# Optimization experiments

Measured on AMD Instinct MI355X. Metric: run time of the kernel, lower is better.

Reference implementation:

```python
import jax, jax.numpy as jnp
import numpy as np

S = 3000    # number of candidate spans (rows of g_i)
P = 80000   # total (mention, antecedent) pairs
GI = 768    # gi_dim
DD = 20     # distance/genre/speaker embedding dim
HID = 150   # mlp hidden dim (fixed in source)
ORDER = 2   # N: one higher-order refinement pass


def setup_inputs() -> dict:
    key = jax.random.key(0)
    ks = jax.random.split(key, 18)
    gij = 3 * GI + 3 * DD
    g_i = jax.random.normal(ks[0], (S, GI), jnp.float32)
    mention_scores = jax.random.normal(ks[1], (S, 1), jnp.float32)
    # sorted segment ids: ragged antecedent counts per mention, grouped contiguously
    mention_ids = jnp.sort(jax.random.randint(ks[2], (P,), 0, S, dtype=jnp.int32))
    antecedent_ids = jax.random.randint(ks[3], (P,), 0, S, dtype=jnp.int32)
    dist_bins = jax.random.randint(ks[4], (P,), 0, 10, dtype=jnp.int32)
    genre_ids = jax.random.randint(ks[5], (P,), 0, 7, dtype=jnp.int32) + 1   # 1..7, 0 is padding_idx
    speaker_ids = jax.random.randint(ks[6], (P,), 0, 2, dtype=jnp.int32) + 1  # 1..2, 0 is padding_idx
    w = lambda k, shp: 0.02 * jax.random.normal(k, shp, jnp.float32)
    dist_emb = w(ks[7], (10, DD))
    genre_emb = w(ks[8], (8, DD)).at[0].set(0.0)     # padding_idx=0
    speaker_emb = w(ks[9], (3, DD)).at[0].set(0.0)   # padding_idx=0
    W1 = w(ks[10], (gij, HID)); b1 = jnp.zeros((HID,), jnp.float32)
    W2 = w(ks[11], (HID, HID)); b2 = jnp.zeros((HID,), jnp.float32)
    W3 = w(ks[12], (HID, 1)); b3 = jnp.zeros((1,), jnp.float32)
    Wf = w(ks[13], (2 * GI, 1)); bf = jnp.zeros((1,), jnp.float32)
    return {"g_i": g_i, "mention_scores": mention_scores, "mention_ids": mention_ids,
            "antecedent_ids": antecedent_ids, "dist_bins": dist_bins, "genre_ids": genre_ids,
            "speaker_ids": speaker_ids, "dist_emb": dist_emb, "genre_emb": genre_emb,
            "speaker_emb": speaker_emb, "W1": W1, "b1": b1, "W2": W2, "b2": b2,
            "W3": W3, "b3": b3, "Wf": Wf, "bf": bf}


def _mlp(x, W1, b1, W2, b2, W3, b3):
    h = jax.nn.relu(x @ W1 + b1)
    h = jax.nn.relu(h @ W2 + b2)
    return h @ W3 + b3


def reference(g_i, mention_scores, mention_ids, antecedent_ids, dist_bins, genre_ids,
              speaker_ids, dist_emb, genre_emb, speaker_emb, W1, b1, W2, b2, W3, b3, Wf, bf):
    phi = jnp.concatenate([dist_emb[dist_bins], genre_emb[genre_ids], speaker_emb[speaker_ids]], axis=1)  # [P,60]
    seg = dict(num_segments=S, indices_are_sorted=True)
    g = g_i
    scores = None
    for n in range(ORDER):
        i_g = g[mention_ids]                # [P,GI] gather
        j_g = g[antecedent_ids]             # [P,GI] gather
        pairs = jnp.concatenate([i_g, j_g, i_g * j_g, phi], axis=1)  # [P,gij]
        scores = _mlp(pairs, W1, b1, W2, b2, W3, b3)                 # [P,1]
        if n < ORDER - 1:
            # higher_order_refinement: ragged segment softmax + weighted scatter update
            s = scores[:, 0]
            seg_max = jax.ops.segment_max(s, mention_ids, **seg)
            safe_max = jnp.where(jnp.isfinite(seg_max), seg_max, 0.0)
            e = jnp.exp(s - safe_max[mention_ids])
            denom = jax.ops.segment_sum(e, mention_ids, **seg)
            attn = e / jnp.where(denom > 0, denom, 1.0)[mention_ids]
            weighted = jax.ops.segment_sum(attn[:, None] * j_g, mention_ids, **seg)  # [S,GI]
            counts = jax.ops.segment_sum(jnp.ones_like(s), mention_ids, **seg)
            f = jax.nn.sigmoid(jnp.concatenate([g, weighted], axis=1) @ Wf + bf)  # [S,1]
            # NOTE: faithful to the source bug: f * mention_id (the integer index), not f * mention_g
            ids_f = jnp.arange(S, dtype=g.dtype)[:, None]
            g_new = f * ids_f + (1.0 - f) * weighted
            g = jnp.where(counts[:, None] > 0, g_new, g)
    s_i = mention_scores[mention_ids]
    s_j = mention_scores[antecedent_ids]
    coref_scores = s_i + s_j + scores       # [P,1]
    # segment softmax with an extra epsilon (score 0) logit per mention
    c = coref_scores[:, 0]
    seg_max = jax.ops.segment_max(c, mention_ids, **seg)
    m = jnp.maximum(jnp.where(jnp.isfinite(seg_max), seg_max, 0.0), 0.0)  # include epsilon logit 0
    e = jnp.exp(c - m[mention_ids])
    denom = jax.ops.segment_sum(e, mention_ids, **seg) + jnp.exp(-m)
    pair_probs = e / denom[mention_ids]     # [P]
    eps_probs = jnp.exp(-m) / denom         # [S]
    return coref_scores, pair_probs, eps_probs
```

## Files before the change

kernel.cpp:

```cpp
#include <hip/hip_runtime.h>

#define GI   768
#define HID  150
#define HPAD 160
#define DDIM 20

typedef __attribute__((ext_vector_type(8))) short v8s;
typedef __attribute__((ext_vector_type(4))) float f32x4;
typedef __attribute__((ext_vector_type(16))) float f32x16;

#define MFMA(A, B, C)   __builtin_amdgcn_mfma_f32_32x32x16_bf16(A, B, C, 0, 0, 0)
#define MFMA16(A, B, C) __builtin_amdgcn_mfma_f32_16x16x32_bf16(A, B, C, 0, 0, 0)

__device__ __forceinline__ ushort bf16rn(float x) {
  unsigned u = __float_as_uint(x);
  return (ushort)((u + 0x7fffu + ((u >> 16) & 1u)) >> 16);
}
__device__ __forceinline__ void bsplit(float x, ushort& h, ushort& l) {
  h = bf16rn(x);
  float fh = __uint_as_float((unsigned)h << 16);
  l = bf16rn(x - fh);
}
__device__ __forceinline__ void tsplit(float x, ushort& h, ushort& l) {
  unsigned u = __float_as_uint(x);
  h = (ushort)(u >> 16);
  float d = x - __uint_as_float(u & 0xffff0000u);
  l = (ushort)(__float_as_uint(d) >> 16);
}
__device__ __forceinline__ uint4 pack8(const ushort* v) {
  uint4 r;
  r.x = v[0] | ((unsigned)v[1] << 16); r.y = v[2] | ((unsigned)v[3] << 16);
  r.z = v[4] | ((unsigned)v[5] << 16); r.w = v[6] | ((unsigned)v[7] << 16);
  return r;
}
__device__ __forceinline__ v8s mk8(const ushort* v) {
  union { uint4 u; v8s s; } t;
  t.u = pack8(v);
  return t.s;
}

__global__ void seg_kernel(const int* __restrict__ mI, int* __restrict__ segs,
                           int P, int S) {
  int m = blockIdx.x * 256 + threadIdx.x;
  if (m > S) return;
  int lo = 0, hi = P;
  while (lo < hi) { int mid = (lo + hi) >> 1; if (mI[mid] < m) lo = mid + 1; else hi = mid; }
  segs[m] = lo;
}

__global__ void phi_kernel(const float* __restrict__ de, const float* __restrict__ ge,
                           const float* __restrict__ se, const float* __restrict__ W1,
                           float* __restrict__ phiW) {
  int idx = blockIdx.x * 256 + threadIdx.x;
  if (idx >= 21 * HPAD) return;
  int row = idx / HPAD, h = idx % HPAD;
  float v = 0.f;
  if (h < HID) {
    const float* emb; int off;
    if (row < 10)      { emb = de + row * DDIM;        off = 0; }
    else if (row < 18) { emb = ge + (row - 10) * DDIM; off = DDIM; }
    else               { emb = se + (row - 18) * DDIM; off = 2 * DDIM; }
    for (int k = 0; k < DDIM; ++k) v += emb[k] * W1[(3 * GI + off + k) * HID + h];
  }
  phiW[row * HPAD + h] = v;
}

#define NWB  (5 * 48 * 512)
#define NW16 (20 * 24 * 512)
#define NW2B (5 * 10 * 512)
__global__ void pad2_kernel(const float* __restrict__ W1, const float* __restrict__ W2,
                            const float* __restrict__ b1, const float* __restrict__ b2,
                            const float* __restrict__ W3,
                            ushort* __restrict__ WBhi, ushort* __restrict__ WBlo,
                            ushort* __restrict__ W16hi, ushort* __restrict__ W16lo,
                            ushort* __restrict__ W2Bhi, ushort* __restrict__ W2Blo,
                            float* __restrict__ b1p, float2* __restrict__ b2w3) {
  int idx = blockIdx.x * 256 + threadIdx.x;
  if (idx < NWB) {
    int c = idx / (48 * 512); int r1 = idx % (48 * 512);
    int s = r1 / 512; int r2 = r1 % 512;
    int l = r2 / 8, j = r2 % 8;
    int h = c * 32 + (l & 31);
    int k = s * 16 + 8 * (l >> 5) + j;
    float x = (h < HID) ? W1[(size_t)(2 * GI + k) * HID + h] : 0.f;
    ushort hh, ll; bsplit(x, hh, ll);
    WBhi[idx] = hh; WBlo[idx] = ll; return;
  }
  idx -= NWB;
  if (idx < NW16) {
    int ct = idx / (24 * 512); int r1 = idx % (24 * 512);
    int s = r1 / 512; int r2 = r1 % 512;
    int l = r2 / 8, j = r2 % 8;
    int col = ct * 16 + (l & 15);
    int k = s * 32 + 8 * (l >> 4) + j;
    int seg = col / HPAD, h = col % HPAD;
    float x = (h < HID) ? W1[(size_t)(seg * GI + k) * HID + h] : 0.f;
    ushort hh, ll; bsplit(x, hh, ll);
    W16hi[idx] = hh; W16lo[idx] = ll; return;
  }
  idx -= NW16;
  if (idx < NW2B) {
    int rt = idx / (10 * 512); int r1 = idx % (10 * 512);
    int s = r1 / 512; int r2 = r1 % 512;
    int l = r2 / 8, j = r2 % 8;
    int h2 = rt * 32 + (l & 31);
    int k = s * 16 + 8 * (l >> 5) + j;
    float x = (k < HID && h2 < HID) ? W2[(size_t)k * HID + h2] : 0.f;
    ushort hh, ll; bsplit(x, hh, ll);
    W2Bhi[idx] = hh; W2Blo[idx] = ll; return;
  }
  idx -= NW2B;
  if (idx < HPAD) { b1p[idx] = (idx < HID) ? b1[idx] : 0.f; return; }
  idx -= HPAD;
  if (idx < HPAD) {
    b2w3[idx] = make_float2((idx < HID) ? b2[idx] : 0.f, (idx < HID) ? W3[idx] : 0.f);
    return;
  }
}

__global__ __launch_bounds__(64, 4) void pre3_kernel(
    const float* __restrict__ g, const ushort* __restrict__ W16hi,
    const ushort* __restrict__ W16lo, float* __restrict__ pre, int S) {
  const int lane = threadIdx.x;
  const int ct = blockIdx.x;
  const int row0 = blockIdx.y * 16;
  int srow = row0 + (lane & 15); if (srow >= S) srow = S - 1;
  const float* gp = g + (size_t)srow * GI + 8 * (lane >> 4);
  const ushort* wph = W16hi + ((size_t)ct * 24 * 64 + lane) * 8;
  const ushort* wpl = W16lo + ((size_t)ct * 24 * 64 + lane) * 8;

  f32x4 acc = {};
#pragma unroll 2
  for (int s = 0; s < 24; ++s) {
    const float4 a0 = *(const float4*)(gp + s * 32);
    const float4 a1 = *(const float4*)(gp + s * 32 + 4);
    const v8s bh = *(const v8s*)(wph + (size_t)s * 512);
    const v8s bl = *(const v8s*)(wpl + (size_t)s * 512);
    float xr[8] = {a0.x, a0.y, a0.z, a0.w, a1.x, a1.y, a1.z, a1.w};
    ushort hs[8], ls[8];
#pragma unroll
    for (int j = 0; j < 8; ++j) tsplit(xr[j], hs[j], ls[j]);
    const v8s ah = mk8(hs), al = mk8(ls);
    acc = MFMA16(ah, bh, acc);
    acc = MFMA16(al, bh, acc);
    acc = MFMA16(ah, bl, acc);
  }
  const int col = ct * 16 + (lane & 15);
#pragma unroll
  for (int r = 0; r < 4; ++r) {
    int sr = row0 + (lane >> 4) * 4 + r;
    if (sr < S) pre[(size_t)sr * 320 + col] = acc[r];
  }
}

__global__ __launch_bounds__(64, 2) void h1a_kernel(
    const float* __restrict__ g, const float* __restrict__ pre,
    const float* __restrict__ phiW,
    const ushort* __restrict__ WBhi, const ushort* __restrict__ WBlo,
    const float* __restrict__ b1p,
    const int* __restrict__ mI, const int* __restrict__ aI,
    const int* __restrict__ db, const int* __restrict__ ge, const int* __restrict__ sp,
    ushort* __restrict__ h1hi, ushort* __restrict__ h1lo, int P) {
  const int lane = threadIdx.x;
  const int lcol = lane & 31, half = lane >> 5;

  const int nwg = gridDim.x;
  const int orig = blockIdx.x;
  const int xcd = orig & 7, idx8 = orig >> 3;
  const int qq = nwg >> 3, rr = nwg & 7;
  const int wg = (xcd < rr ? xcd * (qq + 1) : rr * (qq + 1) + (xcd - rr) * qq) + idx8;
  const int p0 = wg * 32;

  const int myp = p0 + lcol;
  const int iA = mI[myp], jA = aI[myp];
  const int rdL = db[myp], rgL = 10 + ge[myp], rsL = 18 + sp[myp];

  const float* gi = g + (size_t)iA * GI + 8 * half;
  const float* gj = g + (size_t)jA * GI + 8 * half;

  f32x16 acc[5];
  {
    f32x16 z = {};
#pragma unroll
    for (int c = 0; c < 5; ++c) acc[c] = z;
  }

  float4 A0 = *(const float4*)(gi);
  float4 A1 = *(const float4*)(gi + 4);
  float4 B0 = *(const float4*)(gj);
  float4 B1 = *(const float4*)(gj + 4);
  v8s wh[5], wl[5];
#pragma unroll
  for (int c = 0; c < 5; ++c) {
    const size_t o = ((size_t)(c * 48) * 64 + lane) * 8;
    wh[c] = *(const v8s*)(WBhi + o);
    wl[c] = *(const v8s*)(WBlo + o);
  }

#pragma unroll 2
  for (int s = 0; s < 48; ++s) {
    const int sn = (s < 47) ? s + 1 : 47;
    const int dn = sn * 16;
    const float4 nA0 = *(const float4*)(gi + dn);
    const float4 nA1 = *(const float4*)(gi + dn + 4);
    const float4 nB0 = *(const float4*)(gj + dn);
    const float4 nB1 = *(const float4*)(gj + dn + 4);
    v8s nwh[5], nwl[5];
#pragma unroll
    for (int c = 0; c < 5; ++c) {
      const size_t o = ((size_t)(c * 48 + sn) * 64 + lane) * 8;
      nwh[c] = *(const v8s*)(WBhi + o);
      nwl[c] = *(const v8s*)(WBlo + o);
    }
    float xr[8] = {A0.x * B0.x, A0.y * B0.y, A0.z * B0.z, A0.w * B0.w,
                   A1.x * B1.x, A1.y * B1.y, A1.z * B1.z, A1.w * B1.w};
    ushort hs[8], ls[8];
#pragma unroll
    for (int j = 0; j < 8; ++j) tsplit(xr[j], hs[j], ls[j]);
    const v8s ah = mk8(hs), al = mk8(ls);
#pragma unroll
    for (int c = 0; c < 5; ++c) {
      acc[c] = MFMA(ah, wh[c], acc[c]);
      acc[c] = MFMA(al, wh[c], acc[c]);
      acc[c] = MFMA(ah, wl[c], acc[c]);
    }
    A0 = nA0; A1 = nA1; B0 = nB0; B1 = nB1;
#pragma unroll
    for (int c = 0; c < 5; ++c) { wh[c] = nwh[c]; wl[c] = nwl[c]; }
  }

#pragma unroll
  for (int q = 0; q < 16; ++q) {
    const int rr2 = (q & 3) + 8 * (q >> 2) + 4 * half;
    const int pI = __shfl(iA, rr2);
    const int pJ = __shfl(jA, rr2);
    const int rd = __shfl(rdL, rr2), rg = __shfl(rgL, rr2), rs = __shfl(rsL, rr2);
    const float* preI = pre + (size_t)pI * 320;
    const float* preJ = pre + (size_t)pJ * 320 + 160;
    const size_t prow = (size_t)(p0 + rr2) * 160;
#pragma unroll
    for (int c = 0; c < 5; ++c) {
      const int col = c * 32 + lcol;
      float v = acc[c][q] + b1p[col] + preI[col] + preJ[col]
              + phiW[rd * HPAD + col] + phiW[rg * HPAD + col] + phiW[rs * HPAD + col];
      v = fmaxf(v, 0.f);
      ushort hh, ll; tsplit(v, hh, ll);
      h1hi[prow + col] = hh;
      h1lo[prow + col] = ll;
    }
  }
}

__global__ __launch_bounds__(64, 3) void score3_kernel(
    const ushort* __restrict__ h1hi, const ushort* __restrict__ h1lo,
    const ushort* __restrict__ W2Bhi, const ushort* __restrict__ W2Blo,
    const float2* __restrict__ b2w3, const float* __restrict__ b3,
    float* __restrict__ sOut, int P) {
  const int lane = threadIdx.x;
  const int lcol = lane & 31, half = lane >> 5;
  const int p0 = blockIdx.x * 32;

  const ushort* hh = h1hi + (size_t)(p0 + lcol) * 160 + 8 * half;
  const ushort* hl = h1lo + (size_t)(p0 + lcol) * 160 + 8 * half;

  f32x16 acc[5];
  {
    f32x16 z = {};
#pragma unroll
    for (int r = 0; r < 5; ++r) acc[r] = z;
  }

#pragma unroll 2
  for (int s = 0; s < 10; ++s) {
    const v8s bh = *(const v8s*)(hh + s * 16);
    const v8s bl = *(const v8s*)(hl + s * 16);
#pragma unroll
    for (int r = 0; r < 5; ++r) {
      const size_t o = ((size_t)(r * 10 + s) * 64 + lane) * 8;
      const v8s ah = *(const v8s*)(W2Bhi + o);
      const v8s al = *(const v8s*)(W2Blo + o);
      acc[r] = MFMA(ah, bh, acc[r]);
      acc[r] = MFMA(al, bh, acc[r]);
      acc[r] = MFMA(ah, bl, acc[r]);
    }
  }

  float part = 0.f;
#pragma unroll
  for (int r = 0; r < 5; ++r) {
#pragma unroll
    for (int q = 0; q < 16; ++q) {
      const int h2 = r * 32 + (q & 3) + 8 * (q >> 2) + 4 * half;
      const float2 bw = b2w3[h2];
      part += fmaxf(acc[r][q] + bw.x, 0.f) * bw.y;
    }
  }
  part += __shfl_xor(part, 32);
  if (lane < 32) sOut[p0 + lane] = part + b3[0];
}

__global__ void mid_kernel(const float* __restrict__ g, const float* __restrict__ s1,
                           const int* __restrict__ segs, const int* __restrict__ aI,
                           const float* __restrict__ Wf, const float* __restrict__ bf,
                           float* __restrict__ g2) {
  const int m = blockIdx.x;
  const int t = threadIdx.x;
  const int st = segs[m], en = segs[m + 1], n = en - st;
  if (n == 0) {
    for (int d = t; d < GI; d += 256) g2[m * GI + d] = g[m * GI + d];
    return;
  }
  __shared__ float red[256];
  float mx = -INFINITY;
  for (int p = st + t; p < en; p += 256) mx = fmaxf(mx, s1[p]);
  red[t] = mx; __syncthreads();
  for (int s = 128; s > 0; s >>= 1) { if (t < s) red[t] = fmaxf(red[t], red[t + s]); __syncthreads(); }
  mx = red[0]; __syncthreads();
  float sm = 0.f;
  for (int p = st + t; p < en; p += 256) sm += expf(s1[p] - mx);
  red[t] = sm; __syncthreads();
  for (int s = 128; s > 0; s >>= 1) { if (t < s) red[t] += red[t + s]; __syncthreads(); }
  const float denom = red[0]; __syncthreads();
  float wv[3] = {0.f, 0.f, 0.f};
  for (int p = st; p < en; ++p) {
    float e = expf(s1[p] - mx);
    const float* gj = g + (size_t)aI[p] * GI;
#pragma unroll
    for (int u = 0; u < 3; ++u) wv[u] += e * gj[t + u * 256];
  }
#pragma unroll
  for (int u = 0; u < 3; ++u) wv[u] /= denom;
  float part = 0.f;
#pragma unroll
  for (int u = 0; u < 3; ++u) {
    int d = t + u * 256;
    part += g[m * GI + d] * Wf[d] + wv[u] * Wf[GI + d];
  }
  red[t] = part; __syncthreads();
  for (int s = 128; s > 0; s >>= 1) { if (t < s) red[t] += red[t + s]; __syncthreads(); }
  const float f = 1.f / (1.f + expf(-(red[0] + bf[0])));
#pragma unroll
  for (int u = 0; u < 3; ++u) {
    int d = t + u * 256;
    g2[m * GI + d] = f * (float)m + (1.f - f) * wv[u];
  }
}

__global__ void coref_kernel(const float* __restrict__ ms, const float* __restrict__ s2,
                             const int* __restrict__ mI, const int* __restrict__ aI,
                             float* __restrict__ out, int P) {
  int p = blockIdx.x * 256 + threadIdx.x;
  if (p >= P) return;
  out[p] = ms[mI[p]] + ms[aI[p]] + s2[p];
}

__global__ void final_kernel(const float* __restrict__ c, const int* __restrict__ segs,
                             float* __restrict__ pairP, float* __restrict__ epsP) {
  const int m = blockIdx.x;
  const int t = threadIdx.x;
  const int st = segs[m], en = segs[m + 1], n = en - st;
  __shared__ float red[256];
  float mx = -INFINITY;
  for (int p = st + t; p < en; p += 256) mx = fmaxf(mx, c[p]);
  red[t] = mx; __syncthreads();
  for (int s = 128; s > 0; s >>= 1) { if (t < s) red[t] = fmaxf(red[t], red[t + s]); __syncthreads(); }
  mx = red[0]; __syncthreads();
  const float m2 = (n > 0) ? fmaxf(mx, 0.f) : 0.f;
  float sm = 0.f;
  for (int p = st + t; p < en; p += 256) sm += expf(c[p] - m2);
  red[t] = sm; __syncthreads();
  for (int s = 128; s > 0; s >>= 1) { if (t < s) red[t] += red[t + s]; __syncthreads(); }
  const float denom = red[0] + expf(-m2);
  for (int p = st + t; p < en; p += 256) pairP[p] = expf(c[p] - m2) / denom;
  if (t == 0) epsP[m] = expf(-m2) / denom;
}

extern "C" void kernel_launch(void* const* d_in, const int* in_sizes, int n_in,
                              void* d_out, int out_size, void* d_ws, size_t ws_size,
                              hipStream_t stream) {
  const float* g_i  = (const float*)d_in[0];
  const float* ms   = (const float*)d_in[1];
  const int*   mI   = (const int*)d_in[2];
  const int*   aI   = (const int*)d_in[3];
  const int*   db   = (const int*)d_in[4];
  const int*   ge   = (const int*)d_in[5];
  const int*   sp   = (const int*)d_in[6];
  const float* de   = (const float*)d_in[7];
  const float* gemb = (const float*)d_in[8];
  const float* semb = (const float*)d_in[9];
  const float* W1   = (const float*)d_in[10];
  const float* b1   = (const float*)d_in[11];
  const float* W2   = (const float*)d_in[12];
  const float* b2   = (const float*)d_in[13];
  const float* W3   = (const float*)d_in[14];
  const float* b3   = (const float*)d_in[15];
  const float* Wf   = (const float*)d_in[16];
  const float* bf   = (const float*)d_in[17];

  const int S = in_sizes[0] / GI;
  const int P = in_sizes[2];
  float* out = (float*)d_out;

  char* ws = (char*)d_ws;
  size_t off = 0;
  auto take = [&](size_t bytes) -> char* {
    char* p = ws + off;
    off = (off + bytes + 15) & ~(size_t)15;
    return p;
  };
  int*    segs  = (int*)   take((size_t)(S + 1) * 4);
  float*  phiW  = (float*) take((size_t)21 * HPAD * 4);
  float*  pre   = (float*) take((size_t)S * 320 * 4);
  float*  g2    = (float*) take((size_t)S * GI * 4);
  float*  s1    = (float*) take((size_t)P * 4);
  float*  s2    = (float*) take((size_t)P * 4);
  ushort* WBhi  = (ushort*)take((size_t)NWB * 2);
  ushort* WBlo  = (ushort*)take((size_t)NWB * 2);
  ushort* W16hi = (ushort*)take((size_t)NW16 * 2);
  ushort* W16lo = (ushort*)take((size_t)NW16 * 2);
  ushort* W2Bhi = (ushort*)take((size_t)NW2B * 2);
  ushort* W2Blo = (ushort*)take((size_t)NW2B * 2);
  float*  b1p   = (float*) take((size_t)HPAD * 4);
  float2* b2w3  = (float2*)take((size_t)HPAD * 8);
  ushort* h1hi  = (ushort*)take((size_t)P * 160 * 2);
  ushort* h1lo  = (ushort*)take((size_t)P * 160 * 2);

  const int gridSeg = (S + 1 + 255) / 256;
  const int gridPhi = (21 * HPAD + 255) / 256;
  const int padTot  = NWB + NW16 + NW2B + 2 * HPAD;
  const int gridPad = (padTot + 255) / 256;
  const dim3 gridPre(20, (S + 15) / 16);
  const int gridH   = P / 32;
  const int gridCor = (P + 255) / 256;

  seg_kernel<<<gridSeg, 256, 0, stream>>>(mI, segs, P, S);
  phi_kernel<<<gridPhi, 256, 0, stream>>>(de, gemb, semb, W1, phiW);
  pad2_kernel<<<gridPad, 256, 0, stream>>>(W1, W2, b1, b2, W3, WBhi, WBlo,
                                           W16hi, W16lo, W2Bhi, W2Blo, b1p, b2w3);

  pre3_kernel<<<gridPre, 64, 0, stream>>>(g_i, W16hi, W16lo, pre, S);
  h1a_kernel<<<gridH, 64, 0, stream>>>(g_i, pre, phiW, WBhi, WBlo, b1p,
                                       mI, aI, db, ge, sp, h1hi, h1lo, P);
  score3_kernel<<<gridH, 64, 0, stream>>>(h1hi, h1lo, W2Bhi, W2Blo, b2w3, b3, s1, P);
  mid_kernel<<<S, 256, 0, stream>>>(g_i, s1, segs, aI, Wf, bf, g2);

  pre3_kernel<<<gridPre, 64, 0, stream>>>(g2, W16hi, W16lo, pre, S);
  h1a_kernel<<<gridH, 64, 0, stream>>>(g2, pre, phiW, WBhi, WBlo, b1p,
                                       mI, aI, db, ge, sp, h1hi, h1lo, P);
  score3_kernel<<<gridH, 64, 0, stream>>>(h1hi, h1lo, W2Bhi, W2Blo, b2w3, b3, s2, P);

  coref_kernel<<<gridCor, 256, 0, stream>>>(ms, s2, mI, aI, out, P);
  final_kernel<<<S, 256, 0, stream>>>(out, segs, out + P, out + 2 * (size_t)P);
}
```

Baseline: 495.6 us.

## Share staged W1 slices across four waves via LDS; parallelize mid_kernel weighted sum

The pairwise first-layer kernel now runs four waves per block (128 pairs), so weights are loaded once per block into double-buffered LDS with global_load_lds, not separately by every 64-thread block. To support this, the weight layout is interleaved into a single hi/lo array. The mid kernel now splits the antecedent loop across four thread groups with 12 dims each and reduces through shared memory, replacing the serial per-pair loop. The h1 kernel pays a block barrier every k-step and loses register prefetch of g rows, and the extra LDS may limit occupancy.

```diff
diff --git a/kernel.cpp b/kernel.cpp
--- a/kernel.cpp
+++ b/kernel.cpp
@@ -37,6 +37,12 @@
   union { uint4 u; v8s s; } t;
   t.u = pack8(v);
   return t.s;
+}
+
+__device__ __forceinline__ void stage16(const ushort* gsrc, ushort* ldst) {
+  __builtin_amdgcn_global_load_lds(
+      (const __attribute__((address_space(1))) unsigned int*)(const void*)gsrc,
+      (__attribute__((address_space(3))) unsigned int*)(void*)ldst, 16, 0, 0);
 }
 
 __global__ void seg_kernel(const int* __restrict__ mI, int* __restrict__ segs,
@@ -65,28 +71,29 @@
   phiW[row * HPAD + h] = v;
 }
 
-#define NWB  (5 * 48 * 512)
+#define NWS  (48 * 10 * 512)
 #define NW16 (20 * 24 * 512)
 #define NW2B (5 * 10 * 512)
 __global__ void pad2_kernel(const float* __restrict__ W1, const float* __restrict__ W2,
                             const float* __restrict__ b1, const float* __restrict__ b2,
                             const float* __restrict__ W3,
-                            ushort* __restrict__ WBhi, ushort* __restrict__ WBlo,
+                            ushort* __restrict__ WS,
                             ushort* __restrict__ W16hi, ushort* __restrict__ W16lo,
                             ushort* __restrict__ W2Bhi, ushort* __restrict__ W2Blo,
                             float* __restrict__ b1p, float2* __restrict__ b2w3) {
   int idx = blockIdx.x * 256 + threadIdx.x;
-  if (idx < NWB) {
-    int c = idx / (48 * 512); int r1 = idx % (48 * 512);
-    int s = r1 / 512; int r2 = r1 % 512;
+  if (idx < NWS) {
+    int s = idx / (10 * 512); int r1 = idx % (10 * 512);
+    int fi = r1 / 512; int r2 = r1 % 512;
     int l = r2 / 8, j = r2 % 8;
+    int c = fi >> 1, hl = fi & 1;
     int h = c * 32 + (l & 31);
     int k = s * 16 + 8 * (l >> 5) + j;
     float x = (h < HID) ? W1[(size_t)(2 * GI + k) * HID + h] : 0.f;
     ushort hh, ll; bsplit(x, hh, ll);
-    WBhi[idx] = hh; WBlo[idx] = ll; return;
-  }
-  idx -= NWB;
+    WS[idx] = hl ? ll : hh; return;
+  }
+  idx -= NWS;
   if (idx < NW16) {
     int ct = idx / (24 * 512); int r1 = idx % (24 * 512);
     int s = r1 / 512; int r2 = r1 % 512;
@@ -153,30 +160,35 @@
   }
 }
 
-__global__ __launch_bounds__(64, 2) void h1a_kernel(
+__global__ __launch_bounds__(256, 3) void h1b_kernel(
     const float* __restrict__ g, const float* __restrict__ pre,
-    const float* __restrict__ phiW,
-    const ushort* __restrict__ WBhi, const ushort* __restrict__ WBlo,
+    const float* __restrict__ phiW, const ushort* __restrict__ WS,
     const float* __restrict__ b1p,
     const int* __restrict__ mI, const int* __restrict__ aI,
     const int* __restrict__ db, const int* __restrict__ ge, const int* __restrict__ sp,
     ushort* __restrict__ h1hi, ushort* __restrict__ h1lo, int P) {
-  const int lane = threadIdx.x;
+  __shared__ ushort wbuf[2][10 * 512];
+
+  const int t = threadIdx.x;
+  const int lane = t & 63, wv = t >> 6;
   const int lcol = lane & 31, half = lane >> 5;
 
   const int nwg = gridDim.x;
   const int orig = blockIdx.x;
   const int xcd = orig & 7, idx8 = orig >> 3;
-  const int qq = nwg >> 3, rr = nwg & 7;
-  const int wg = (xcd < rr ? xcd * (qq + 1) : rr * (qq + 1) + (xcd - rr) * qq) + idx8;
-  const int p0 = wg * 32;
-
-  const int myp = p0 + lcol;
+  const int qq = nwg >> 3, rq = nwg & 7;
+  const int wg = (xcd < rq ? xcd * (qq + 1) : rq * (qq + 1) + (xcd - rq) * qq) + idx8;
+  const int p0w = wg * 128 + wv * 32;
+
+  const int myp = p0w + lcol;
   const int iA = mI[myp], jA = aI[myp];
   const int rdL = db[myp], rgL = 10 + ge[myp], rsL = 18 + sp[myp];
 
   const float* gi = g + (size_t)iA * GI + 8 * half;
   const float* gj = g + (size_t)jA * GI + 8 * half;
+
+  const int f0 = 2 * wv, f1 = 2 * wv + 1;
+  const int f2 = (wv < 2) ? 8 + wv : -1;
 
   f32x16 acc[5];
   {
@@ -185,48 +197,48 @@
     for (int c = 0; c < 5; ++c) acc[c] = z;
   }
 
-  float4 A0 = *(const float4*)(gi);
-  float4 A1 = *(const float4*)(gi + 4);
-  float4 B0 = *(const float4*)(gj);
-  float4 B1 = *(const float4*)(gj + 4);
-  v8s wh[5], wl[5];
-#pragma unroll
-  for (int c = 0; c < 5; ++c) {
-    const size_t o = ((size_t)(c * 48) * 64 + lane) * 8;
-    wh[c] = *(const v8s*)(WBhi + o);
-    wl[c] = *(const v8s*)(WBlo + o);
-  }
-
+  {
+    const ushort* base = WS + (size_t)0 * 10 * 512;
+    stage16(base + f0 * 512 + lane * 8, &wbuf[0][f0 * 512]);
+    stage16(base + f1 * 512 + lane * 8, &wbuf[0][f1 * 512]);
+    if (f2 >= 0) stage16(base + f2 * 512 + lane * 8, &wbuf[0][f2 * 512]);
+  }
+  asm volatile("s_waitcnt vmcnt(0)" ::: "memory");
+  __syncthreads();
+
+  int cur = 0;
 #pragma unroll 2
   for (int s = 0; s < 48; ++s) {
-    const int sn = (s < 47) ? s + 1 : 47;
-    const int dn = sn * 16;
-    const float4 nA0 = *(const float4*)(gi + dn);
-    const float4 nA1 = *(const float4*)(gi + dn + 4);
-    const float4 nB0 = *(const float4*)(gj + dn);
-    const float4 nB1 = *(const float4*)(gj + dn + 4);
-    v8s nwh[5], nwl[5];
-#pragma unroll
-    for (int c = 0; c < 5; ++c) {
-      const size_t o = ((size_t)(c * 48 + sn) * 64 + lane) * 8;
-      nwh[c] = *(const v8s*)(WBhi + o);
-      nwl[c] = *(const v8s*)(WBlo + o);
+    if (s + 1 < 48) {
+      const ushort* base = WS + (size_t)(s + 1) * 10 * 512;
+      ushort* dst = wbuf[cur ^ 1];
+      stage16(base + f0 * 512 + lane * 8, dst + f0 * 512);
+      stage16(base + f1 * 512 + lane * 8, dst + f1 * 512);
+      if (f2 >= 0) stage16(base + f2 * 512 + lane * 8, dst + f2 * 512);
     }
-    float xr[8] = {A0.x * B0.x, A0.y * B0.y, A0.z * B0.z, A0.w * B0.w,
-                   A1.x * B1.x, A1.y * B1.y, A1.z * B1.z, A1.w * B1.w};
+    const int d0 = s * 16;
+    const float4 a0 = *(const float4*)(gi + d0);
+    const float4 a1 = *(const float4*)(gi + d0 + 4);
+    const float4 b0 = *(const float4*)(gj + d0);
+    const float4 b1v = *(const float4*)(gj + d0 + 4);
+    float xr[8] = {a0.x * b0.x, a0.y * b0.y, a0.z * b0.z, a0.w * b0.w,
+                   a1.x * b1v.x, a1.y * b1v.y, a1.z * b1v.z, a1.w * b1v.w};
     ushort hs[8], ls[8];
 #pragma unroll
     for (int j = 0; j < 8; ++j) tsplit(xr[j], hs[j], ls[j]);
     const v8s ah = mk8(hs), al = mk8(ls);
+    const ushort* wb = wbuf[cur];
 #pragma unroll
     for (int c = 0; c < 5; ++c) {
-      acc[c] = MFMA(ah, wh[c], acc[c]);
-      acc[c] = MFMA(al, wh[c], acc[c]);
-      acc[c] = MFMA(ah, wl[c], acc[c]);
+      const v8s wh = *(const v8s*)(wb + (2 * c) * 512 + lane * 8);
+      const v8s wl = *(const v8s*)(wb + (2 * c + 1) * 512 + lane * 8);
+      acc[c] = MFMA(ah, wh, acc[c]);
+      acc[c] = MFMA(al, wh, acc[c]);
+      acc[c] = MFMA(ah, wl, acc[c]);
     }
-    A0 = nA0; A1 = nA1; B0 = nB0; B1 = nB1;
-#pragma unroll
-    for (int c = 0; c < 5; ++c) { wh[c] = nwh[c]; wl[c] = nwl[c]; }
+    asm volatile("s_waitcnt vmcnt(0)" ::: "memory");
+    __syncthreads();
+    cur ^= 1;
   }
 
 #pragma unroll
@@ -237,7 +249,7 @@
     const int rd = __shfl(rdL, rr2), rg = __shfl(rgL, rr2), rs = __shfl(rsL, rr2);
     const float* preI = pre + (size_t)pI * 320;
     const float* preJ = pre + (size_t)pJ * 320 + 160;
-    const size_t prow = (size_t)(p0 + rr2) * 160;
+    const size_t prow = (size_t)(p0w + rr2) * 160;
 #pragma unroll
     for (int c = 0; c < 5; ++c) {
       const int col = c * 32 + lcol;
@@ -311,38 +323,46 @@
     return;
   }
   __shared__ float red[256];
+  __shared__ float wred[4][GI];
   float mx = -INFINITY;
   for (int p = st + t; p < en; p += 256) mx = fmaxf(mx, s1[p]);
   red[t] = mx; __syncthreads();
   for (int s = 128; s > 0; s >>= 1) { if (t < s) red[t] = fmaxf(red[t], red[t + s]); __syncthreads(); }
   mx = red[0]; __syncthreads();
-  float sm = 0.f;
-  for (int p = st + t; p < en; p += 256) sm += expf(s1[p] - mx);
-  red[t] = sm; __syncthreads();
+  const int dg = t & 63, pg = t >> 6;
+  float wv[12];
+#pragma unroll
+  for (int u = 0; u < 12; ++u) wv[u] = 0.f;
+  float esum = 0.f;
+  for (int p = st + pg; p < en; p += 4) {
+    const float e = expf(s1[p] - mx);
+    esum += e;
+    const float* gj = g + (size_t)aI[p] * GI + dg;
+#pragma unroll
+    for (int u = 0; u < 12; ++u) wv[u] += e * gj[u * 64];
+  }
+  red[t] = (dg == 0) ? esum : 0.f; __syncthreads();
   for (int s = 128; s > 0; s >>= 1) { if (t < s) red[t] += red[t + s]; __syncthreads(); }
   const float denom = red[0]; __syncthreads();
-  float wv[3] = {0.f, 0.f, 0.f};
-  for (int p = st; p < en; ++p) {
-    float e = expf(s1[p] - mx);
-    const float* gj = g + (size_t)aI[p] * GI;
-#pragma unroll
-    for (int u = 0; u < 3; ++u) wv[u] += e * gj[t + u * 256];
-  }
-#pragma unroll
-  for (int u = 0; u < 3; ++u) wv[u] /= denom;
+#pragma unroll
+  for (int u = 0; u < 12; ++u) wred[pg][dg + u * 64] = wv[u];
+  __syncthreads();
   float part = 0.f;
+  float wfin[3];
 #pragma unroll
   for (int u = 0; u < 3; ++u) {
-    int d = t + u * 256;
-    part += g[m * GI + d] * Wf[d] + wv[u] * Wf[GI + d];
+    const int d = t + u * 256;
+    float ws = (wred[0][d] + wred[1][d] + wred[2][d] + wred[3][d]) / denom;
+    wfin[u] = ws;
+    part += g[(size_t)m * GI + d] * Wf[d] + ws * Wf[GI + d];
   }
   red[t] = part; __syncthreads();
   for (int s = 128; s > 0; s >>= 1) { if (t < s) red[t] += red[t + s]; __syncthreads(); }
   const float f = 1.f / (1.f + expf(-(red[0] + bf[0])));
 #pragma unroll
   for (int u = 0; u < 3; ++u) {
-    int d = t + u * 256;
-    g2[m * GI + d] = f * (float)m + (1.f - f) * wv[u];
+    const int d = t + u * 256;
+    g2[(size_t)m * GI + d] = f * (float)m + (1.f - f) * wfin[u];
   }
 }
 
@@ -414,8 +434,7 @@
   float*  g2    = (float*) take((size_t)S * GI * 4);
   float*  s1    = (float*) take((size_t)P * 4);
   float*  s2    = (float*) take((size_t)P * 4);
-  ushort* WBhi  = (ushort*)take((size_t)NWB * 2);
-  ushort* WBlo  = (ushort*)take((size_t)NWB * 2);
+  ushort* WS    = (ushort*)take((size_t)NWS * 2);
   ushort* W16hi = (ushort*)take((size_t)NW16 * 2);
   ushort* W16lo = (ushort*)take((size_t)NW16 * 2);
   ushort* W2Bhi = (ushort*)take((size_t)NW2B * 2);
@@ -427,27 +446,28 @@
 
   const int gridSeg = (S + 1 + 255) / 256;
   const int gridPhi = (21 * HPAD + 255) / 256;
-  const int padTot  = NWB + NW16 + NW2B + 2 * HPAD;
+  const int padTot  = NWS + NW16 + NW2B + 2 * HPAD;
   const int gridPad = (padTot + 255) / 256;
   const dim3 gridPre(20, (S + 15) / 16);
-  const int gridH   = P / 32;
+  const int gridH   = P / 128;
+  const int gridS3  = P / 32;
   const int gridCor = (P + 255) / 256;
 
   seg_kernel<<<gridSeg, 256, 0, stream>>>(mI, segs, P, S);
   phi_kernel<<<gridPhi, 256, 0, stream>>>(de, gemb, semb, W1, phiW);
-  pad2_kernel<<<gridPad, 256, 0, stream>>>(W1, W2, b1, b2, W3, WBhi, WBlo,
+  pad2_kernel<<<gridPad, 256, 0, stream>>>(W1, W2, b1, b2, W3, WS,
                                            W16hi, W16lo, W2Bhi, W2Blo, b1p, b2w3);
 
   pre3_kernel<<<gridPre, 64, 0, stream>>>(g_i, W16hi, W16lo, pre, S);
-  h1a_kernel<<<gridH, 64, 0, stream>>>(g_i, pre, phiW, WBhi, WBlo, b1p,
-                                       mI, aI, db, ge, sp, h1hi, h1lo, P);
-  score3_kernel<<<gridH, 64, 0, stream>>>(h1hi, h1lo, W2Bhi, W2Blo, b2w3, b3, s1, P);
+  h1b_kernel<<<gridH, 256, 0, stream>>>(g_i, pre, phiW, WS, b1p,
+                                        mI, aI, db, ge, sp, h1hi, h1lo, P);
+  score3_kernel<<<gridS3, 64, 0, stream>>>(h1hi, h1lo, W2Bhi, W2Blo, b2w3, b3, s1, P);
   mid_kernel<<<S, 256, 0, stream>>>(g_i, s1, segs, aI, Wf, bf, g2);
 
   pre3_kernel<<<gridPre, 64, 0, stream>>>(g2, W16hi, W16lo, pre, S);
-  h1a_kernel<<<gridH, 64, 0, stream>>>(g2, pre, phiW, WBhi, WBlo, b1p,
-                                       mI, aI, db, ge, sp, h1hi, h1lo, P);
-  score3_kernel<<<gridH, 64, 0, stream>>>(h1hi, h1lo, W2Bhi, W2Blo, b2w3, b3, s2, P);
+  h1b_kernel<<<gridH, 256, 0, stream>>>(g2, pre, phiW, WS, b1p,
+                                        mI, aI, db, ge, sp, h1hi, h1lo, P);
+  score3_kernel<<<gridS3, 64, 0, stream>>>(h1hi, h1lo, W2Bhi, W2Blo, b2w3, b3, s2, P);
 
   coref_kernel<<<gridCor, 256, 0, stream>>>(ms, s2, mI, aI, out, P);
   final_kernel<<<S, 256, 0, stream>>>(out, segs, out + P, out + 2 * (size_t)P);
```

Result: faster. 472.3 us (-4.7%).
